# Kernel optimization log

Hardware: AMD Instinct MI355X
Metric: run time of the kernel (lower is better)

Reference implementation:

```python
import jax, jax.numpy as jnp
import numpy as np

B, Q, G = 32, 4000, 100
C1, C2, C3 = 4, 32, 8
ALPHA, GAMMA = 0.25, 2.0
OTA_K = 5
CENTER_RADIUS = 2.5
COST_BBOX = 1.0
COST_GIOU = 1.0
COST_CLASS = 1.0 / 3.0  # forward sets self.cost_class = 1/len(heads) = 1/3


def box_xyxy_to_cxcywh(b):
    x0, y0, x1, y1 = b[..., 0], b[..., 1], b[..., 2], b[..., 3]
    return jnp.stack([(x0 + x1) * 0.5, (y0 + y1) * 0.5, x1 - x0, y1 - y0], axis=-1)


def box_cxcywh_to_xyxy(b):
    cx, cy, w, h = b[..., 0], b[..., 1], b[..., 2], b[..., 3]
    return jnp.stack([cx - 0.5 * w, cy - 0.5 * h, cx + 0.5 * w, cy + 0.5 * h], axis=-1)


def box_iou(a, b):
    # a [Q,4], b [G,4] in xyxy -> iou, union [Q,G]
    area_a = (a[:, 2] - a[:, 0]) * (a[:, 3] - a[:, 1])
    area_b = (b[:, 2] - b[:, 0]) * (b[:, 3] - b[:, 1])
    lt = jnp.maximum(a[:, None, :2], b[None, :, :2])
    rb = jnp.minimum(a[:, None, 2:], b[None, :, 2:])
    wh = jnp.clip(rb - lt, 0.0)
    inter = wh[..., 0] * wh[..., 1]
    union = area_a[:, None] + area_b[None, :] - inter
    return inter / union, union


def generalized_box_iou(a, b):
    iou, union = box_iou(a, b)
    lt = jnp.minimum(a[:, None, :2], b[None, :, :2])
    rb = jnp.maximum(a[:, None, 2:], b[None, :, 2:])
    wh = jnp.clip(rb - lt, 0.0)
    area = wh[..., 0] * wh[..., 1]
    return iou - (area - union) / area


def get_in_boxes_info(boxes_c, gts_c):
    # boxes_c [Q,4] cxcywh anchors, gts_c [G,4] cxcywh gts
    xy = box_cxcywh_to_xyxy(gts_c)  # [G,4]
    ax, ay = boxes_c[:, 0:1], boxes_c[:, 1:2]  # [Q,1]
    in_box = (ax > xy[:, 0]) & (ax < xy[:, 2]) & (ay > xy[:, 1]) & (ay < xy[:, 3])  # [Q,G]
    w = xy[:, 2] - xy[:, 0]
    h = xy[:, 3] - xy[:, 1]
    cx, cy = gts_c[:, 0], gts_c[:, 1]
    in_ctr = ((ax > cx - CENTER_RADIUS * w) & (ax < cx + CENTER_RADIUS * w) &
              (ay > cy - CENTER_RADIUS * h) & (ay < cy + CENTER_RADIUS * h))
    fg_mask = jnp.any(in_box, axis=1) | jnp.any(in_ctr, axis=1)  # [Q]
    return fg_mask, in_box & in_ctr


def compute_cost(l1, l2, l3, pb, gb, isz, t1, t2, t3):
    fg_mask, in_bc = get_in_boxes_info(box_xyxy_to_cxcywh(pb), box_xyxy_to_cxcywh(gb))
    ious, _ = box_iou(pb, gb)

    def focal_cost(logits, labels):
        p = jax.nn.sigmoid(logits)
        neg = (1.0 - ALPHA) * p ** GAMMA * (-jnp.log(1.0 - p + 1e-8))
        pos = ALPHA * (1.0 - p) ** GAMMA * (-jnp.log(p + 1e-8))
        return (pos - neg)[:, labels]  # [Q,G]

    cc = focal_cost(l1, t1) + focal_cost(l2, t2) + focal_cost(l3, t3)
    nb = pb / isz[None, :]
    ng = gb / isz[None, :]
    cost_bbox = jnp.sum(jnp.abs(nb[:, None, :] - ng[None, :, :]), axis=-1)  # L1 cdist [Q,G]
    cost_giou = -generalized_box_iou(pb, gb)
    cost = (COST_BBOX * cost_bbox + COST_CLASS * cc + COST_GIOU * cost_giou
            + 100.0 * (~in_bc).astype(cost_bbox.dtype))
    cost = cost + 10000.0 * (~fg_mask)[:, None].astype(cost.dtype)
    return cost, ious


def dynamic_k_matching(cost, ious):
    q, g = cost.shape
    topk_ious, _ = jax.lax.top_k(ious.T, OTA_K)  # [G,k]
    dynamic_ks = jnp.clip(topk_ious.sum(1).astype(jnp.int32), 1, None)  # [G]
    # top dynamic_ks[g] lowest-cost queries per gt (dynamic_ks <= OTA_K since ious in [0,1])
    _, pos_idx = jax.lax.top_k(-cost.T, OTA_K)  # [G,k]
    valid = (jnp.arange(OTA_K)[None, :] < dynamic_ks[:, None]).astype(cost.dtype)
    m = jnp.zeros_like(cost).at[pos_idx, jnp.arange(g)[:, None]].add(valid)

    def resolve(m_, c_):
        # anchors matched to >1 gt keep only their min-cost gt
        multi = m_.sum(1) > 1
        one = jax.nn.one_hot(jnp.argmin(c_, axis=1), g, dtype=m_.dtype)
        return jnp.where(multi[:, None], one, m_)

    m = resolve(m, cost)

    def cond(st):
        return jnp.any(st[0].sum(0) == 0)

    def body(st):
        m_, c_ = st
        c_ = c_ + jnp.where((m_.sum(1) > 0)[:, None], 1e5, 0.0)  # penalize already-matched queries
        unmatched = m_.sum(0) == 0  # [G]
        one = jax.nn.one_hot(jnp.argmin(c_, axis=0), q, dtype=m_.dtype, axis=0)  # [Q,G]
        m_ = jnp.where(unmatched[None, :], one, m_)
        m_ = resolve(m_, c_)
        return (m_, c_)

    m, c = jax.lax.while_loop(cond, body, (m, cost))
    selected = m.sum(1) > 0            # [Q] bool: which queries are matched
    gt_idx = jnp.argmax(m, axis=1)     # [Q] gt index per query (valid where selected)
    matched_qidx = jnp.argmin(jnp.where(m > 0, c, jnp.inf), axis=0)  # [G]
    return m, selected, gt_idx, matched_qidx


def reference(pred_logits_1, pred_logits_2, pred_logits_3, pred_boxes, gt_boxes_xyxy, img_size, labels_1, labels_2, labels_3):
    def per_image(l1, l2, l3, pb, gb, isz, t1, t2, t3):
        cost, ious = compute_cost(l1, l2, l3, pb, gb, isz, t1, t2, t3)
        m, selected, gt_idx, matched_qidx = dynamic_k_matching(cost, ious)
        return m, selected, gt_idx, matched_qidx, cost
    return jax.vmap(per_image)(pred_logits_1, pred_logits_2, pred_logits_3,
                               pred_boxes, gt_boxes_xyxy, img_size,
                               labels_1, labels_2, labels_3)


def setup_inputs() -> dict:
    key = jax.random.key(0)
    ks = jax.random.split(key, 8)

    def rand_boxes(k, n):
        k1, k2 = jax.random.split(k)
        cxcy = jax.random.uniform(k1, (B, n, 2), minval=32.0, maxval=480.0)
        wh = jax.random.uniform(k2, (B, n, 2), minval=16.0, maxval=128.0)
        return jnp.concatenate([cxcy - wh * 0.5, cxcy + wh * 0.5], axis=-1)

    return {
        "pred_logits_1": jax.random.normal(ks[0], (B, Q, C1), jnp.float32),
        "pred_logits_2": jax.random.normal(ks[1], (B, Q, C2), jnp.float32),
        "pred_logits_3": jax.random.normal(ks[2], (B, Q, C3), jnp.float32),
        "pred_boxes": rand_boxes(ks[3], Q),
        "gt_boxes_xyxy": rand_boxes(ks[4], G),
        "img_size": jnp.full((B, 4), 512.0, jnp.float32),
        "labels_1": jax.random.randint(ks[5], (B, G), 0, C1),
        "labels_2": jax.random.randint(ks[6], (B, G), 0, C2),
        "labels_3": jax.random.randint(ks[7], (B, G), 0, C3),
    }
```

## Files before the change

### kernel.cpp

```cpp
#include <hip/hip_runtime.h>
#include <math.h>
#include <stdint.h>

#define NB 32
#define NQ 4000
#define NG 100
#define NC1 4
#define NC2 32
#define NC3 8
#define NCT 44
#define SLK 16
#define MTH 512
#define QB  128

static const size_t OFF_M    = 0;
static const size_t OFF_SEL  = (size_t)NB * NQ * NG;
static const size_t OFF_GTI  = OFF_SEL + (size_t)NB * NQ;
static const size_t OFF_MQ   = OFF_GTI + (size_t)NB * NQ;
static const size_t OFF_COST = OFF_MQ + (size_t)NB * NG;

__device__ __forceinline__ float focal_diff(float x) {
    float p   = 1.0f / (1.0f + expf(-x));
    float neg = 0.75f * (p * p) * (-logf(1.0f - p + 1e-8f));
    float pos = 0.25f * ((1.0f - p) * (1.0f - p)) * (-logf(p + 1e-8f));
    return pos - neg;
}

__device__ __forceinline__ unsigned ordered_bits(float f) {
    unsigned u = __float_as_uint(f);
    return (u & 0x80000000u) ? ~u : (u | 0x80000000u);
}

__global__ __launch_bounds__(256) void focal_kernel(
    const float* __restrict__ l1, const float* __restrict__ l2, const float* __restrict__ l3,
    float* __restrict__ FDT)
{
    const int b  = blockIdx.y;
    const int q0 = blockIdx.x * 64;
    const int tid = threadIdx.x;
    __shared__ float tile[64][NCT + 1];

    for (int idx = tid; idx < 64 * NC1; idx += 256) {
        const int qi = idx >> 2, c = idx & 3;
        const int q = q0 + qi;
        if (q < NQ) tile[qi][c] = focal_diff(l1[((size_t)b * NQ + q) * NC1 + c]);
    }
    for (int idx = tid; idx < 64 * NC2; idx += 256) {
        const int qi = idx >> 5, c = idx & 31;
        const int q = q0 + qi;
        if (q < NQ) tile[qi][NC1 + c] = focal_diff(l2[((size_t)b * NQ + q) * NC2 + c]);
    }
    for (int idx = tid; idx < 64 * NC3; idx += 256) {
        const int qi = idx >> 3, c = idx & 7;
        const int q = q0 + qi;
        if (q < NQ) tile[qi][NC1 + NC2 + c] = focal_diff(l3[((size_t)b * NQ + q) * NC3 + c]);
    }
    __syncthreads();

    for (int idx = tid; idx < NCT * 64; idx += 256) {
        const int c = idx >> 6, qi = idx & 63;
        const int q = q0 + qi;
        if (q < NQ) FDT[((size_t)b * NCT + c) * NQ + q] = tile[qi][c];
    }
}

__global__ __launch_bounds__(256) void mask_kernel(
    const float* __restrict__ pb, const float* __restrict__ gbx,
    uint4* __restrict__ bmout, float* __restrict__ fgout)
{
    const int b   = blockIdx.y;
    const int tid = threadIdx.x;

    __shared__ float s_ib[NG][4];
    __shared__ float s_ic[NG][4];

    if (tid < NG) {
        const int g = tid;
        const float x0 = gbx[((size_t)b * NG + g) * 4 + 0];
        const float y0 = gbx[((size_t)b * NG + g) * 4 + 1];
        const float x1 = gbx[((size_t)b * NG + g) * 4 + 2];
        const float y1 = gbx[((size_t)b * NG + g) * 4 + 3];
        const float cx = (x0 + x1) * 0.5f, cy = (y0 + y1) * 0.5f;
        const float w0 = x1 - x0, h0 = y1 - y0;
        const float bx0 = cx - 0.5f * w0, bx1 = cx + 0.5f * w0;
        const float by0 = cy - 0.5f * h0, by1 = cy + 0.5f * h0;
        s_ib[g][0] = bx0; s_ib[g][1] = by0; s_ib[g][2] = bx1; s_ib[g][3] = by1;
        const float w = bx1 - bx0, h = by1 - by0;
        s_ic[g][0] = cx - 2.5f * w; s_ic[g][1] = cx + 2.5f * w;
        s_ic[g][2] = cy - 2.5f * h; s_ic[g][3] = cy + 2.5f * h;
    }
    __syncthreads();

    const int q = blockIdx.x * 256 + tid;
    if (q >= NQ) return;

    const float4 pv = reinterpret_cast<const float4*>(pb)[(size_t)b * NQ + q];
    const float ax = (pv.x + pv.z) * 0.5f, ay = (pv.y + pv.w) * 0.5f;

    unsigned bm[4] = {0u, 0u, 0u, 0u};
    bool fg = false;
    for (int g = 0; g < NG; ++g) {
        const bool ib = (ax > s_ib[g][0]) && (ax < s_ib[g][2]) && (ay > s_ib[g][1]) && (ay < s_ib[g][3]);
        const bool ic = (ax > s_ic[g][0]) && (ax < s_ic[g][1]) && (ay > s_ic[g][2]) && (ay < s_ic[g][3]);
        fg = fg || ib || ic;
        if (ib && ic) bm[g >> 5] |= (1u << (g & 31));
    }
    bmout[(size_t)b * NQ + q] = make_uint4(bm[0], bm[1], bm[2], bm[3]);
    fgout[(size_t)b * NQ + q] = fg ? 0.0f : 10000.0f;
}

__global__ __launch_bounds__(256) void cost_kernel(
    const float* __restrict__ pb, const float* __restrict__ gbx, const float* __restrict__ img,
    const int* __restrict__ t1, const int* __restrict__ t2, const int* __restrict__ t3,
    const float* __restrict__ FDT, const uint4* __restrict__ bmin, const float* __restrict__ fgin,
    float* __restrict__ costT, float* __restrict__ outc)
{
    const int b   = blockIdx.y;
    const int q0  = blockIdx.x * QB;
    const int tid = threadIdx.x;
    const int qi  = tid & (QB - 1);
    const int hf  = tid >> 7;

    __shared__ float s_ng[NG][4];
    __shared__ float s_gx[NG][4];
    __shared__ float s_ab[NG];
    __shared__ int   s_lab[NG][3];
    __shared__ float s_isz[4];
    __shared__ float tile[QB][NG + 1];

    if (tid < 4) s_isz[tid] = img[b * 4 + tid];
    if (tid < NG) {
        const int g = tid;
        const float x0 = gbx[((size_t)b * NG + g) * 4 + 0];
        const float y0 = gbx[((size_t)b * NG + g) * 4 + 1];
        const float x1 = gbx[((size_t)b * NG + g) * 4 + 2];
        const float y1 = gbx[((size_t)b * NG + g) * 4 + 3];
        s_gx[g][0] = x0; s_gx[g][1] = y0; s_gx[g][2] = x1; s_gx[g][3] = y1;
        s_ab[g] = (x1 - x0) * (y1 - y0);
        s_ng[g][0] = x0 / img[b * 4 + 0];
        s_ng[g][1] = y0 / img[b * 4 + 1];
        s_ng[g][2] = x1 / img[b * 4 + 2];
        s_ng[g][3] = y1 / img[b * 4 + 3];
        s_lab[g][0] = t1[b * NG + g];
        s_lab[g][1] = NC1 + t2[b * NG + g];
        s_lab[g][2] = NC1 + NC2 + t3[b * NG + g];
    }
    __syncthreads();

    const int q = q0 + qi;
    if (q < NQ) {
        const float4 pv = reinterpret_cast<const float4*>(pb)[(size_t)b * NQ + q];
        const float p0 = pv.x, p1 = pv.y, p2 = pv.z, p3 = pv.w;
        const float areaA = (p2 - p0) * (p3 - p1);
        const float n0 = p0 / s_isz[0], n1 = p1 / s_isz[1], n2 = p2 / s_isz[2], n3 = p3 / s_isz[3];

        const uint4 bm4 = bmin[(size_t)b * NQ + q];
        const unsigned bm[4] = {bm4.x, bm4.y, bm4.z, bm4.w};
        const float fgadd = fgin[(size_t)b * NQ + q];

        const float* F = FDT + (size_t)b * NCT * NQ + q;
        float* ct = costT + (size_t)b * NG * NQ + q;
        const int gbeg = hf * (NG / 2);
#pragma unroll 5
        for (int gl = 0; gl < NG / 2; ++gl) {
            const int g = gbeg + gl;
            const float f1 = F[(size_t)s_lab[g][0] * NQ];
            const float f2 = F[(size_t)s_lab[g][1] * NQ];
            const float f3 = F[(size_t)s_lab[g][2] * NQ];
            float cb = fabsf(n0 - s_ng[g][0]);
            cb = cb + fabsf(n1 - s_ng[g][1]);
            cb = cb + fabsf(n2 - s_ng[g][2]);
            cb = cb + fabsf(n3 - s_ng[g][3]);
            const float gx0 = s_gx[g][0], gy0 = s_gx[g][1], gx1 = s_gx[g][2], gy1 = s_gx[g][3];
            const float ltx = fmaxf(p0, gx0), lty = fmaxf(p1, gy0);
            const float rbx = fminf(p2, gx1), rby = fminf(p3, gy1);
            const float iw = fmaxf(rbx - ltx, 0.0f), ih = fmaxf(rby - lty, 0.0f);
            const float inter = iw * ih;
            const float uni = areaA + s_ab[g] - inter;
            const float iou = inter / uni;
            const float ex0 = fminf(p0, gx0), ey0 = fminf(p1, gy0);
            const float ex1 = fmaxf(p2, gx1), ey1 = fmaxf(p3, gy1);
            const float ew = fmaxf(ex1 - ex0, 0.0f), eh = fmaxf(ey1 - ey0, 0.0f);
            const float ea = ew * eh;
            const float giou = iou - (ea - uni) / ea;
            const float cc = (f1 + f2) + f3;
            const bool inbc = (bm[g >> 5] >> (g & 31)) & 1u;
            float cost = cb;
            cost = cost + 0.33333334f * cc;
            cost = cost + (-giou);
            cost = cost + (inbc ? 0.0f : 100.0f);
            cost = cost + fgadd;
            ct[(size_t)g * NQ] = cost;
            tile[qi][g] = cost;
        }
    }
    __syncthreads();

    const int nrows = (NQ - q0 < QB) ? (NQ - q0) : QB;
    float4* OCb = reinterpret_cast<float4*>(outc + ((size_t)b * NQ + q0) * NG);
    for (int idx = tid; idx < nrows * (NG / 4); idx += 256) {
        const int r = idx / (NG / 4), j = idx - r * (NG / 4);
        float4 v;
        v.x = tile[r][4 * j + 0];
        v.y = tile[r][4 * j + 1];
        v.z = tile[r][4 * j + 2];
        v.w = tile[r][4 * j + 3];
        OCb[(size_t)r * (NG / 4) + j] = v;
    }
}

template <bool MAXSEL>
__device__ __forceinline__ bool better(float av, int ai, float bv, int bi) {
    if (MAXSEL) return (av > bv) || (av == bv && ai < bi);
    else        return (av < bv) || (av == bv && ai < bi);
}

template <bool MAXSEL>
__device__ __forceinline__ void ins5(float (&v)[5], int (&id)[5], float nv, int ni) {
    if (!better<MAXSEL>(nv, ni, v[4], id[4])) return;
    v[4] = nv; id[4] = ni;
#pragma unroll
    for (int j = 4; j > 0; --j) {
        if (better<MAXSEL>(v[j], id[j], v[j - 1], id[j - 1])) {
            float tv = v[j]; v[j] = v[j - 1]; v[j - 1] = tv;
            int   ti = id[j]; id[j] = id[j - 1]; id[j - 1] = ti;
        }
    }
}

template <bool MAXSEL>
__device__ __forceinline__ void merge5(float (&v)[5], int (&id)[5], float (&ov)[5], int (&oi)[5]) {
#pragma unroll
    for (int r = 0; r < 5; ++r) {
        float bv = v[0]; int bi = id[0];
#pragma unroll
        for (int off = 32; off >= 1; off >>= 1) {
            float xv = __shfl_xor(bv, off, 64);
            int   xi = __shfl_xor(bi, off, 64);
            if (better<MAXSEL>(xv, xi, bv, bi)) { bv = xv; bi = xi; }
        }
        ov[r] = bv; oi[r] = bi;
        if (id[0] == bi) {
            v[0] = v[1]; id[0] = id[1];
            v[1] = v[2]; id[1] = id[2];
            v[2] = v[3]; id[2] = id[3];
            v[3] = v[4]; id[3] = id[4];
            v[4] = MAXSEL ? -INFINITY : INFINITY; id[4] = 0x7fffffff;
        }
    }
}

__device__ __forceinline__ void push_max5i(float (&v)[5], int (&id)[5], float t, int it) {
#pragma unroll
    for (int i = 0; i < 5; ++i) {
        const bool b = t > v[i];
        const float nv = b ? t : v[i];
        const float nt = b ? v[i] : t;
        const int ni  = b ? it : id[i];
        const int nit = b ? id[i] : it;
        v[i] = nv; id[i] = ni; t = nt; it = nit;
    }
}

#define CHUNK 1000

#define CE(i, j) { const unsigned long long _a = kk[i], _b = kk[j]; \
                   const bool _s = _b < _a; \
                   kk[i] = _s ? _b : _a; kk[j] = _s ? _a : _b; }

__global__ __launch_bounds__(256, 2) void col_topk_kernel(
    const float* __restrict__ pb, const float* __restrict__ gbx, const float* __restrict__ costT,
    int* __restrict__ grc, int* __restrict__ grnew, int* __restrict__ grsl)
{
    const int g = blockIdx.x, b = blockIdx.y;
    const int tid = threadIdx.x, lane = tid & 63, wave = tid >> 6;

    __shared__ float              s_v[4][5];
    __shared__ int                s_i[4][5];
    __shared__ unsigned long long s_ck[4][SLK];

    const float gx0 = gbx[((size_t)b * NG + g) * 4 + 0];
    const float gy0 = gbx[((size_t)b * NG + g) * 4 + 1];
    const float gx1 = gbx[((size_t)b * NG + g) * 4 + 2];
    const float gy1 = gbx[((size_t)b * NG + g) * 4 + 3];
    const float areaB = (gx1 - gx0) * (gy1 - gy0);
    const float4* PB = reinterpret_cast<const float4*>(pb) + (size_t)b * NQ;
    const float* CT = costT + (size_t)b * NG * NQ + (size_t)g * NQ;

    const int q0 = wave * CHUNK;

    {
        unsigned long long kk[16];
#pragma unroll
        for (int i = 0; i < 16; ++i) {
            const bool live = (i < 15) || (lane < 40);
            const int q = q0 + i * 64 + lane;
            const float c = live ? CT[q] : 0.0f;
            kk[i] = live ? ((((unsigned long long)ordered_bits(c)) << 32) | (unsigned)q)
                         : ~0ull;
        }

        CE(0,1)  CE(2,3)  CE(4,5)  CE(6,7)  CE(8,9)  CE(10,11) CE(12,13) CE(14,15)
        CE(0,2)  CE(1,3)  CE(4,6)  CE(5,7)  CE(8,10) CE(9,11)  CE(12,14) CE(13,15)
        CE(1,2)  CE(5,6)  CE(9,10) CE(13,14)
        CE(0,4)  CE(1,5)  CE(2,6)  CE(3,7)  CE(8,12) CE(9,13)  CE(10,14) CE(11,15)
        CE(2,4)  CE(3,5)  CE(10,12) CE(11,13)
        CE(1,2)  CE(3,4)  CE(5,6)  CE(9,10) CE(11,12) CE(13,14)
        CE(0,8)  CE(1,9)  CE(2,10) CE(3,11) CE(4,12)  CE(5,13)  CE(6,14)  CE(7,15)
        CE(4,8)  CE(5,9)  CE(6,10) CE(7,11)
        CE(2,4)  CE(3,5)  CE(6,8)  CE(7,9)  CE(10,12) CE(11,13)
        CE(1,2)  CE(3,4)  CE(5,6)  CE(7,8)  CE(9,10)  CE(11,12) CE(13,14)

        for (int r = 0; r < SLK; ++r) {
            unsigned long long bk = kk[0];
#pragma unroll
            for (int off = 32; off >= 1; off >>= 1) {
                const unsigned long long xk = __shfl_xor(bk, off, 64);
                if (xk < bk) bk = xk;
            }
            if (lane == 0) s_ck[wave][r] = bk;
            if (kk[0] == bk) {
#pragma unroll
                for (int j = 0; j < 15; ++j) kk[j] = kk[j + 1];
                kk[15] = ~0ull;
            }
        }
    }

    {
        const int q1 = q0 + CHUNK;
        float tv[5]; int ti[5];
#pragma unroll
        for (int k = 0; k < 5; ++k) { tv[k] = -INFINITY; ti[k] = 0x7fffffff; }
        for (int base = q0; base < q1; base += 64) {
            const int q = base + lane;
            if (q < q1) {
                const float4 p = PB[q];
                const float ltx = fmaxf(p.x, gx0), lty = fmaxf(p.y, gy0);
                const float rbx = fminf(p.z, gx1), rby = fminf(p.w, gy1);
                const float iw = fmaxf(rbx - ltx, 0.0f), ih = fmaxf(rby - lty, 0.0f);
                const float inter = iw * ih;
                const float areaA = (p.z - p.x) * (p.w - p.y);
                const float uni = areaA + areaB - inter;
                push_max5i(tv, ti, inter / uni, q);
            }
        }
        float ov[5]; int oi[5];
        merge5<true>(tv, ti, ov, oi);
        if (lane == 0) {
#pragma unroll
            for (int k = 0; k < 5; ++k) { s_v[wave][k] = ov[k]; s_i[wave][k] = oi[k]; }
        }
    }
    __syncthreads();

    if (tid == 0) {
        float tv[5]; int ti[5];
#pragma unroll
        for (int k = 0; k < 5; ++k) { tv[k] = -INFINITY; ti[k] = 0x7fffffff; }
        for (int w = 0; w < 4; ++w)
#pragma unroll
            for (int k = 0; k < 5; ++k) ins5<true>(tv, ti, s_v[w][k], s_i[w][k]);
        const float s = ((((tv[0] + tv[1]) + tv[2]) + tv[3]) + tv[4]);
        int dk = (int)s;
        if (dk < 1) dk = 1;

        int h0 = 0, h1 = 0, h2 = 0, h3 = 0;
        int* SL = grsl + ((size_t)b * NG + g) * SLK;
        for (int k = 0; k < SLK; ++k) {
            unsigned long long bk = ~0ull; int bw = 0;
            if (h0 < SLK && s_ck[0][h0] < bk) { bk = s_ck[0][h0]; bw = 0; }
            if (h1 < SLK && s_ck[1][h1] < bk) { bk = s_ck[1][h1]; bw = 1; }
            if (h2 < SLK && s_ck[2][h2] < bk) { bk = s_ck[2][h2]; bw = 2; }
            if (h3 < SLK && s_ck[3][h3] < bk) { bk = s_ck[3][h3]; bw = 3; }
            if (bw == 0) h0++; else if (bw == 1) h1++; else if (bw == 2) h2++; else h3++;
            const int bi = (int)(unsigned)(bk & 0xffffffffull);
            SL[k] = bi;
            if (k < dk) {
                atomicAdd(&grc[b * NQ + bi], 1);
                grnew[b * NQ + bi] = g;
            }
        }
    }
}

__device__ __forceinline__ float pen_add(float v, int k) {
    while (k-- > 0) v += 100000.0f;
    return v;
}

__global__ __launch_bounds__(MTH) void match_kernel(
    const float* __restrict__ costT, const int* __restrict__ grc, const int* __restrict__ grnew,
    const int* __restrict__ grsl,
    float* __restrict__ out, int* __restrict__ rm_out)
{
    const int b = blockIdx.x, tid = threadIdx.x;
    const int lane = tid & 63, wave = tid >> 6;

    __shared__ short              rmatch[NQ];
    __shared__ short              rnew[NQ];
    __shared__ short              tmat[NQ];
    __shared__ int                rc[NQ];
    __shared__ int                colc[NG];
    __shared__ unsigned long long colkey[NG];
    __shared__ short              sl[NG * SLK];
    __shared__ short              wl[2][1024];
    __shared__ int                wlc[2];
    __shared__ int                flag;

    const float* CT = costT + (size_t)b * NG * NQ;

    if (tid == 0) { wlc[0] = 0; wlc[1] = 0; }
    if (tid < NG) colc[tid] = 0;
    __syncthreads();

    for (int q = tid; q < NQ; q += MTH) {
        rmatch[q] = -1;
        const int r = grc[b * NQ + q];
        rc[q] = r;
        rnew[q] = (short)grnew[b * NQ + q];
        if (r > 0) { const int i = atomicAdd(&wlc[0], 1); wl[0][i] = (short)q; }
    }
    for (int i = tid; i < NG * SLK; i += MTH) sl[i] = (short)grsl[(size_t)b * NG * SLK + i];
    __syncthreads();

    int L = 2000;
    for (int iter = 0; iter < 2000; ++iter) {
        const int p = iter & 1;
        const int n = wlc[p];
        for (int i = tid; i < n; i += MTH) {
            const int q = (int)wl[p][i];
            const int rcq = atomicExch(&rc[q], 0);
            if (rcq == 0) continue;
            const int oldm = rmatch[q];
            const int c = rcq + (oldm >= 0 ? 1 : 0);
            int nm;
            if (c == 1) nm = (int)rnew[q];
            else {
                const int kp = (oldm >= 0) ? (iter - (int)tmat[q]) : 0;
                float bv = INFINITY; nm = 0;
                for (int g = 0; g < NG; ++g) {
                    const float v = pen_add(CT[(size_t)g * NQ + q], kp);
                    if (v < bv) { bv = v; nm = g; }
                }
            }
            rmatch[q] = (short)nm;
            if (oldm < 0) { tmat[q] = (short)iter; atomicAdd(&colc[nm], 1); }
            else if (oldm != nm) { atomicSub(&colc[oldm], 1); atomicAdd(&colc[nm], 1); }
        }
        if (tid == 0) { wlc[p ^ 1] = 0; flag = 0; }
        __syncthreads();

        for (int g = wave; g < NG; g += (MTH / 64)) {
            if (colc[g] != 0) continue;
            if (lane == 0) flag = 1;
            int cand = -1;
            if (lane < SLK) {
                const int qq = (int)sl[g * SLK + lane];
                if (rmatch[qq] < 0) cand = qq;
            }
            const unsigned long long bal = __ballot(cand >= 0);
            int bi;
            if (bal != 0ull) {
                const int src = __ffsll(bal) - 1;
                bi = __shfl(cand, src, 64);
            } else {
                float bv = INFINITY; bi = 0x7fffffff;
                for (int base = 0; base < NQ; base += 64) {
                    const int q = base + lane;
                    if (q < NQ) {
                        const int kp = (rmatch[q] >= 0) ? (iter + 1 - (int)tmat[q]) : 0;
                        const float v = pen_add(CT[(size_t)g * NQ + q], kp);
                        if (v < bv || (v == bv && q < bi)) { bv = v; bi = q; }
                    }
                }
#pragma unroll
                for (int off = 32; off >= 1; off >>= 1) {
                    const float xv = __shfl_xor(bv, off, 64);
                    const int   xi = __shfl_xor(bi, off, 64);
                    if (xv < bv || (xv == bv && xi < bi)) { bv = xv; bi = xi; }
                }
            }
            if (lane == 0) {
                atomicAdd(&rc[bi], 1);
                rnew[bi] = (short)g;
                const int i = atomicAdd(&wlc[p ^ 1], 1);
                wl[p ^ 1][i] = (short)bi;
            }
        }
        __syncthreads();
        if (!flag) { L = iter; break; }
    }

    if (tid < NG) colkey[tid] = ~0ull;
    __syncthreads();
    for (int q = tid; q < NQ; q += MTH) {
        const int m = rmatch[q];
        out[OFF_SEL + (size_t)b * NQ + q] = (m >= 0) ? 1.0f : 0.0f;
        out[OFF_GTI + (size_t)b * NQ + q] = (float)(m >= 0 ? m : 0);
        rm_out[b * NQ + q] = m;
        if (m >= 0) {
            const float v = pen_add(CT[(size_t)m * NQ + q], L - (int)tmat[q]);
            const unsigned long long key = ((unsigned long long)ordered_bits(v) << 32) | (unsigned)q;
            atomicMin(&colkey[m], key);
        }
    }
    __syncthreads();
    if (tid < NG) out[OFF_MQ + (size_t)b * NG + tid] = (float)(unsigned)(colkey[tid] & 0xffffffffull);
}

__global__ __launch_bounds__(256) void m_expand_kernel(
    const int* __restrict__ rm, float* __restrict__ out)
{
    const int b = blockIdx.y;
    const int q = blockIdx.x * 256 + threadIdx.x;
    if (q >= NQ) return;
    const int m = rm[b * NQ + q];
    float4* OM = reinterpret_cast<float4*>(out + OFF_M + ((size_t)b * NQ + q) * NG);
#pragma unroll
    for (int j = 0; j < NG / 4; ++j) {
        const int g0 = j * 4;
        float4 v;
        v.x = (m == g0 + 0) ? 1.0f : 0.0f;
        v.y = (m == g0 + 1) ? 1.0f : 0.0f;
        v.z = (m == g0 + 2) ? 1.0f : 0.0f;
        v.w = (m == g0 + 3) ? 1.0f : 0.0f;
        OM[j] = v;
    }
}

extern "C" void kernel_launch(void* const* d_in, const int* in_sizes, int n_in,
                              void* d_out, int out_size, void* d_ws, size_t ws_size,
                              hipStream_t stream)
{
    const float* l1  = (const float*)d_in[0];
    const float* l2  = (const float*)d_in[1];
    const float* l3  = (const float*)d_in[2];
    const float* pb  = (const float*)d_in[3];
    const float* gbx = (const float*)d_in[4];
    const float* img = (const float*)d_in[5];
    const int*   t1  = (const int*)d_in[6];
    const int*   t2  = (const int*)d_in[7];
    const int*   t3  = (const int*)d_in[8];
    float* out = (float*)d_out;

    char* ws = (char*)d_ws;
    float* costT = (float*)ws;                                   ws += (size_t)NB * NG * NQ * sizeof(float);
    int*   rm    = (int*)ws;                                     ws += (size_t)NB * NQ * sizeof(int);
    int*   grc   = (int*)ws;                                     ws += (size_t)NB * NQ * sizeof(int);
    int*   grnew = (int*)ws;                                     ws += (size_t)NB * NQ * sizeof(int);
    uint4* bmws  = (uint4*)ws;                                   ws += (size_t)NB * NQ * sizeof(uint4);
    float* fgws  = (float*)ws;                                   ws += (size_t)NB * NQ * sizeof(float);
    int*   grsl  = (int*)ws;

    float* FDT = out + OFF_M;
    float* OC  = out + OFF_COST;

    hipMemsetAsync(grc, 0, (size_t)NB * NQ * sizeof(int), stream);

    dim3 fg((NQ + 63) / 64, NB);
    focal_kernel<<<fg, 256, 0, stream>>>(l1, l2, l3, FDT);

    dim3 mk((NQ + 255) / 256, NB);
    mask_kernel<<<mk, 256, 0, stream>>>(pb, gbx, bmws, fgws);

    dim3 cg((NQ + QB - 1) / QB, NB);
    cost_kernel<<<cg, 256, 0, stream>>>(pb, gbx, img, t1, t2, t3, FDT, bmws, fgws, costT, OC);

    dim3 kg(NG, NB);
    col_topk_kernel<<<kg, 256, 0, stream>>>(pb, gbx, costT, grc, grnew, grsl);

    match_kernel<<<NB, MTH, 0, stream>>>(costT, grc, grnew, grsl, out, rm);

    dim3 wg((NQ + 255) / 256, NB);
    m_expand_kernel<<<wg, 256, 0, stream>>>(rm, out);
}
```

Baseline: 313.5 us.

## Fuse mask into cost kernel and build candidate counts inside match kernel

The separate mask kernel is removed. Each cost thread now computes the in-box and center masks for its half of the ground truths and shares the foreground flag through shared memory. Global atomics and the memset for per-query candidate counts are replaced by shared-memory accumulation in the match kernel, built from the top-k lists and a per-column dynamic-k array. SLK is halved to shrink the stored candidate list; this assumes dynamic k never exceeds 8, which holds when OTA_K is 5.

```diff
diff --git a/kernel.cpp b/kernel.cpp
--- a/kernel.cpp
+++ b/kernel.cpp
@@ -9,7 +9,7 @@
 #define NC2 32
 #define NC3 8
 #define NCT 44
-#define SLK 16
+#define SLK 8
 #define MTH 512
 #define QB  128
 
@@ -64,55 +64,10 @@
     }
 }
 
-__global__ __launch_bounds__(256) void mask_kernel(
-    const float* __restrict__ pb, const float* __restrict__ gbx,
-    uint4* __restrict__ bmout, float* __restrict__ fgout)
-{
-    const int b   = blockIdx.y;
-    const int tid = threadIdx.x;
-
-    __shared__ float s_ib[NG][4];
-    __shared__ float s_ic[NG][4];
-
-    if (tid < NG) {
-        const int g = tid;
-        const float x0 = gbx[((size_t)b * NG + g) * 4 + 0];
-        const float y0 = gbx[((size_t)b * NG + g) * 4 + 1];
-        const float x1 = gbx[((size_t)b * NG + g) * 4 + 2];
-        const float y1 = gbx[((size_t)b * NG + g) * 4 + 3];
-        const float cx = (x0 + x1) * 0.5f, cy = (y0 + y1) * 0.5f;
-        const float w0 = x1 - x0, h0 = y1 - y0;
-        const float bx0 = cx - 0.5f * w0, bx1 = cx + 0.5f * w0;
-        const float by0 = cy - 0.5f * h0, by1 = cy + 0.5f * h0;
-        s_ib[g][0] = bx0; s_ib[g][1] = by0; s_ib[g][2] = bx1; s_ib[g][3] = by1;
-        const float w = bx1 - bx0, h = by1 - by0;
-        s_ic[g][0] = cx - 2.5f * w; s_ic[g][1] = cx + 2.5f * w;
-        s_ic[g][2] = cy - 2.5f * h; s_ic[g][3] = cy + 2.5f * h;
-    }
-    __syncthreads();
-
-    const int q = blockIdx.x * 256 + tid;
-    if (q >= NQ) return;
-
-    const float4 pv = reinterpret_cast<const float4*>(pb)[(size_t)b * NQ + q];
-    const float ax = (pv.x + pv.z) * 0.5f, ay = (pv.y + pv.w) * 0.5f;
-
-    unsigned bm[4] = {0u, 0u, 0u, 0u};
-    bool fg = false;
-    for (int g = 0; g < NG; ++g) {
-        const bool ib = (ax > s_ib[g][0]) && (ax < s_ib[g][2]) && (ay > s_ib[g][1]) && (ay < s_ib[g][3]);
-        const bool ic = (ax > s_ic[g][0]) && (ax < s_ic[g][1]) && (ay > s_ic[g][2]) && (ay < s_ic[g][3]);
-        fg = fg || ib || ic;
-        if (ib && ic) bm[g >> 5] |= (1u << (g & 31));
-    }
-    bmout[(size_t)b * NQ + q] = make_uint4(bm[0], bm[1], bm[2], bm[3]);
-    fgout[(size_t)b * NQ + q] = fg ? 0.0f : 10000.0f;
-}
-
 __global__ __launch_bounds__(256) void cost_kernel(
     const float* __restrict__ pb, const float* __restrict__ gbx, const float* __restrict__ img,
     const int* __restrict__ t1, const int* __restrict__ t2, const int* __restrict__ t3,
-    const float* __restrict__ FDT, const uint4* __restrict__ bmin, const float* __restrict__ fgin,
+    const float* __restrict__ FDT,
     float* __restrict__ costT, float* __restrict__ outc)
 {
     const int b   = blockIdx.y;
@@ -126,6 +81,9 @@
     __shared__ float s_ab[NG];
     __shared__ int   s_lab[NG][3];
     __shared__ float s_isz[4];
+    __shared__ float s_ib[NG][4];
+    __shared__ float s_ic[NG][4];
+    __shared__ short fgh[QB][2];
     __shared__ float tile[QB][NG + 1];
 
     if (tid < 4) s_isz[tid] = img[b * 4 + tid];
@@ -144,23 +102,46 @@
         s_lab[g][0] = t1[b * NG + g];
         s_lab[g][1] = NC1 + t2[b * NG + g];
         s_lab[g][2] = NC1 + NC2 + t3[b * NG + g];
+        const float cx = (x0 + x1) * 0.5f, cy = (y0 + y1) * 0.5f;
+        const float w0 = x1 - x0, h0 = y1 - y0;
+        const float bx0 = cx - 0.5f * w0, bx1 = cx + 0.5f * w0;
+        const float by0 = cy - 0.5f * h0, by1 = cy + 0.5f * h0;
+        s_ib[g][0] = bx0; s_ib[g][1] = by0; s_ib[g][2] = bx1; s_ib[g][3] = by1;
+        const float w = bx1 - bx0, h = by1 - by0;
+        s_ic[g][0] = cx - 2.5f * w; s_ic[g][1] = cx + 2.5f * w;
+        s_ic[g][2] = cy - 2.5f * h; s_ic[g][3] = cy + 2.5f * h;
     }
     __syncthreads();
 
     const int q = q0 + qi;
-    if (q < NQ) {
-        const float4 pv = reinterpret_cast<const float4*>(pb)[(size_t)b * NQ + q];
+    const bool alive = (q < NQ);
+    const int gbeg = hf * (NG / 2);
+
+    float4 pv;
+    unsigned long long bmh = 0ull;
+    short fgloc = 0;
+    if (alive) {
+        pv = reinterpret_cast<const float4*>(pb)[(size_t)b * NQ + q];
+        const float ax = (pv.x + pv.z) * 0.5f, ay = (pv.y + pv.w) * 0.5f;
+        for (int gl = 0; gl < NG / 2; ++gl) {
+            const int g = gbeg + gl;
+            const bool ib = (ax > s_ib[g][0]) && (ax < s_ib[g][2]) && (ay > s_ib[g][1]) && (ay < s_ib[g][3]);
+            const bool ic = (ax > s_ic[g][0]) && (ax < s_ic[g][1]) && (ay > s_ic[g][2]) && (ay < s_ic[g][3]);
+            if (ib || ic) fgloc = 1;
+            if (ib && ic) bmh |= (1ull << gl);
+        }
+    }
+    fgh[qi][hf] = fgloc;
+    __syncthreads();
+
+    if (alive) {
         const float p0 = pv.x, p1 = pv.y, p2 = pv.z, p3 = pv.w;
         const float areaA = (p2 - p0) * (p3 - p1);
         const float n0 = p0 / s_isz[0], n1 = p1 / s_isz[1], n2 = p2 / s_isz[2], n3 = p3 / s_isz[3];
-
-        const uint4 bm4 = bmin[(size_t)b * NQ + q];
-        const unsigned bm[4] = {bm4.x, bm4.y, bm4.z, bm4.w};
-        const float fgadd = fgin[(size_t)b * NQ + q];
+        const float fgadd = (fgh[qi][0] | fgh[qi][1]) ? 0.0f : 10000.0f;
 
         const float* F = FDT + (size_t)b * NCT * NQ + q;
         float* ct = costT + (size_t)b * NG * NQ + q;
-        const int gbeg = hf * (NG / 2);
 #pragma unroll 5
         for (int gl = 0; gl < NG / 2; ++gl) {
             const int g = gbeg + gl;
@@ -184,7 +165,7 @@
             const float ea = ew * eh;
             const float giou = iou - (ea - uni) / ea;
             const float cc = (f1 + f2) + f3;
-            const bool inbc = (bm[g >> 5] >> (g & 31)) & 1u;
+            const bool inbc = (bmh >> gl) & 1ull;
             float cost = cb;
             cost = cost + 0.33333334f * cc;
             cost = cost + (-giou);
@@ -270,7 +251,7 @@
 
 __global__ __launch_bounds__(256, 2) void col_topk_kernel(
     const float* __restrict__ pb, const float* __restrict__ gbx, const float* __restrict__ costT,
-    int* __restrict__ grc, int* __restrict__ grnew, int* __restrict__ grsl)
+    int* __restrict__ grsl, int* __restrict__ grdk)
 {
     const int g = blockIdx.x, b = blockIdx.y;
     const int tid = threadIdx.x, lane = tid & 63, wave = tid >> 6;
@@ -374,13 +355,9 @@
             if (h2 < SLK && s_ck[2][h2] < bk) { bk = s_ck[2][h2]; bw = 2; }
             if (h3 < SLK && s_ck[3][h3] < bk) { bk = s_ck[3][h3]; bw = 3; }
             if (bw == 0) h0++; else if (bw == 1) h1++; else if (bw == 2) h2++; else h3++;
-            const int bi = (int)(unsigned)(bk & 0xffffffffull);
-            SL[k] = bi;
-            if (k < dk) {
-                atomicAdd(&grc[b * NQ + bi], 1);
-                grnew[b * NQ + bi] = g;
-            }
-        }
+            SL[k] = (int)(unsigned)(bk & 0xffffffffull);
+        }
+        grdk[b * NG + g] = dk;
     }
 }
 
@@ -390,8 +367,7 @@
 }
 
 __global__ __launch_bounds__(MTH) void match_kernel(
-    const float* __restrict__ costT, const int* __restrict__ grc, const int* __restrict__ grnew,
-    const int* __restrict__ grsl,
+    const float* __restrict__ costT, const int* __restrict__ grsl, const int* __restrict__ grdk,
     float* __restrict__ out, int* __restrict__ rm_out)
 {
     const int b = blockIdx.x, tid = threadIdx.x;
@@ -404,6 +380,7 @@
     __shared__ int                colc[NG];
     __shared__ unsigned long long colkey[NG];
     __shared__ short              sl[NG * SLK];
+    __shared__ int                sdk[NG];
     __shared__ short              wl[2][1024];
     __shared__ int                wlc[2];
     __shared__ int                flag;
@@ -411,17 +388,25 @@
     const float* CT = costT + (size_t)b * NG * NQ;
 
     if (tid == 0) { wlc[0] = 0; wlc[1] = 0; }
-    if (tid < NG) colc[tid] = 0;
+    if (tid < NG) { colc[tid] = 0; sdk[tid] = grdk[b * NG + tid]; }
+    for (int q = tid; q < NQ; q += MTH) { rmatch[q] = -1; rc[q] = 0; rnew[q] = 0; }
+    for (int i = tid; i < NG * SLK; i += MTH) sl[i] = (short)grsl[(size_t)b * NG * SLK + i];
+    __syncthreads();
+
+    if (tid < NG) {
+        const int g = tid;
+        const int dk = sdk[g];
+        for (int k = 0; k < dk; ++k) {
+            const int q = (int)sl[g * SLK + k];
+            atomicAdd(&rc[q], 1);
+            rnew[q] = (short)g;
+        }
+    }
     __syncthreads();
 
     for (int q = tid; q < NQ; q += MTH) {
-        rmatch[q] = -1;
-        const int r = grc[b * NQ + q];
-        rc[q] = r;
-        rnew[q] = (short)grnew[b * NQ + q];
-        if (r > 0) { const int i = atomicAdd(&wlc[0], 1); wl[0][i] = (short)q; }
-    }
-    for (int i = tid; i < NG * SLK; i += MTH) sl[i] = (short)grsl[(size_t)b * NG * SLK + i];
+        if (rc[q] > 0) { const int i = atomicAdd(&wlc[0], 1); wl[0][i] = (short)q; }
+    }
     __syncthreads();
 
     int L = 2000;
@@ -547,30 +532,22 @@
     char* ws = (char*)d_ws;
     float* costT = (float*)ws;                                   ws += (size_t)NB * NG * NQ * sizeof(float);
     int*   rm    = (int*)ws;                                     ws += (size_t)NB * NQ * sizeof(int);
-    int*   grc   = (int*)ws;                                     ws += (size_t)NB * NQ * sizeof(int);
-    int*   grnew = (int*)ws;                                     ws += (size_t)NB * NQ * sizeof(int);
-    uint4* bmws  = (uint4*)ws;                                   ws += (size_t)NB * NQ * sizeof(uint4);
-    float* fgws  = (float*)ws;                                   ws += (size_t)NB * NQ * sizeof(float);
-    int*   grsl  = (int*)ws;
+    int*   grsl  = (int*)ws;                                     ws += (size_t)NB * NG * SLK * sizeof(int);
+    int*   grdk  = (int*)ws;
 
     float* FDT = out + OFF_M;
     float* OC  = out + OFF_COST;
 
-    hipMemsetAsync(grc, 0, (size_t)NB * NQ * sizeof(int), stream);
-
     dim3 fg((NQ + 63) / 64, NB);
     focal_kernel<<<fg, 256, 0, stream>>>(l1, l2, l3, FDT);
 
-    dim3 mk((NQ + 255) / 256, NB);
-    mask_kernel<<<mk, 256, 0, stream>>>(pb, gbx, bmws, fgws);
-
     dim3 cg((NQ + QB - 1) / QB, NB);
-    cost_kernel<<<cg, 256, 0, stream>>>(pb, gbx, img, t1, t2, t3, FDT, bmws, fgws, costT, OC);
+    cost_kernel<<<cg, 256, 0, stream>>>(pb, gbx, img, t1, t2, t3, FDT, costT, OC);
 
     dim3 kg(NG, NB);
-    col_topk_kernel<<<kg, 256, 0, stream>>>(pb, gbx, costT, grc, grnew, grsl);
-
-    match_kernel<<<NB, MTH, 0, stream>>>(costT, grc, grnew, grsl, out, rm);
+    col_topk_kernel<<<kg, 256, 0, stream>>>(pb, gbx, costT, grsl, grdk);
+
+    match_kernel<<<NB, MTH, 0, stream>>>(costT, grsl, grdk, out, rm);
 
     dim3 wg((NQ + 255) / 256, NB);
     m_expand_kernel<<<wg, 256, 0, stream>>>(rm, out);
```

Result: faster. 294.9 us (-6.0%).
